# Optimization experiments

Hardware: AMD Instinct MI355X
Metric: run time of the kernel (lower is better)

The kernel has to match this reference:

```python
import jax, jax.numpy as jnp
import numpy as np

B, S, D = 2, 2048, 1024
H = 16
DH = D // H


def _layernorm(x, g, b, eps=1e-5):
    mu = jnp.mean(x, axis=-1, keepdims=True)
    var = jnp.var(x, axis=-1, keepdims=True)
    return (x - mu) * jax.lax.rsqrt(var + eps) * g + b


def setup_inputs() -> dict:
    key = jax.random.key(0)
    ks = jax.random.split(key, 8)
    s = lambda fan_in: 1.0 / np.sqrt(fan_in)
    return {
        "x": jax.random.normal(ks[0], (B, S, D), dtype=jnp.float32),
        "ln1_g": jnp.ones((D,), jnp.float32),
        "ln1_b": jnp.zeros((D,), jnp.float32),
        "w_qkv": jax.random.uniform(ks[1], (D, 3 * D), jnp.float32, -s(D), s(D)),
        "b_qkv": jnp.zeros((3 * D,), jnp.float32),
        "w_out": jax.random.uniform(ks[2], (D, D), jnp.float32, -s(D), s(D)),
        "b_out": jnp.zeros((D,), jnp.float32),
        "ln2_g": jnp.ones((D,), jnp.float32),
        "ln2_b": jnp.zeros((D,), jnp.float32),
        "w1": jax.random.uniform(ks[3], (D, 4 * D), jnp.float32, -s(D), s(D)),
        "b1": jnp.zeros((4 * D,), jnp.float32),
        "w2": jax.random.uniform(ks[4], (4 * D, D), jnp.float32, -s(4 * D), s(4 * D)),
        "b2": jnp.zeros((D,), jnp.float32),
    }


def reference(x, ln1_g, ln1_b, w_qkv, b_qkv, w_out, b_out,
              ln2_g, ln2_b, w1, b1, w2, b2):
    scale = DH ** -0.5
    residual = x
    h = _layernorm(x, ln1_g, ln1_b)
    qkv = h @ w_qkv + b_qkv                      # [B,S,3D]
    q, k, v = jnp.split(qkv, 3, axis=-1)
    # [B,S,D] -> [B,H,S,DH]
    split_heads = lambda t: t.reshape(B, S, H, DH).transpose(0, 2, 1, 3)
    q, k, v = map(split_heads, (q, k, v))
    scores = jnp.einsum("bhsd,bhtd->bhst", q, k) * scale  # full O(S^2) matrix
    attn = jax.nn.softmax(scores, axis=-1)
    out = jnp.einsum("bhst,bhtd->bhsd", attn, v)
    out = out.transpose(0, 2, 1, 3).reshape(B, S, D)
    out = out @ w_out + b_out                    # dropout is identity at eval
    x = residual + out
    residual = x
    h = _layernorm(x, ln2_g, ln2_b)
    h = jax.nn.gelu(h @ w1 + b1, approximate=False)
    h = h @ w2 + b2
    return residual + h
```

## Files before the change

### kernel.cpp

```cpp
#include <hip/hip_runtime.h>
#include <hip/hip_bf16.h>
#include <math.h>

#define Bc 2
#define Sc 2048
#define Dc 1024
#define Hc 16
#define DHc 64
#define Mc (Bc*Sc)

typedef __attribute__((ext_vector_type(8))) short bf16x8;
typedef __attribute__((ext_vector_type(4))) float f32x4;

#define QSCALE 0.18033688f

__device__ __forceinline__ ushort f2bf(float f){
  union { float f; uint32_t u; } c; c.f = f;
  uint32_t u = c.u;
  return (ushort)((u + 0x7fffu + ((u >> 16) & 1u)) >> 16);
}
__device__ __forceinline__ float fast_exp2(float x){
#if __has_builtin(__builtin_amdgcn_exp2f)
  return __builtin_amdgcn_exp2f(x);
#else
  return exp2f(x);
#endif
}
__device__ __forceinline__ float fast_rcp(float x){
#if __has_builtin(__builtin_amdgcn_rcpf)
  return __builtin_amdgcn_rcpf(x);
#else
  return 1.0f / x;
#endif
}
__device__ __forceinline__ float fast_gelu(float x){
  float x2 = x * x;
  float y  = x * (2.30220826f + 0.10294442f * x2);
  float t  = fast_exp2(fminf(y, 80.f));
  return x * t * fast_rcp(t + 1.0f);
}
__device__ __forceinline__ uint32_t cvt_pk_bf16(float a, float b){
  uint32_t r;
  asm("v_cvt_pk_bf16_f32 %0, %1, %2" : "=v"(r) : "v"(a), "v"(b));
  return r;
}

__device__ __forceinline__ void stage16(const void* g, void* lbase, int lane){
#if __has_builtin(__builtin_amdgcn_global_load_lds)
  __builtin_amdgcn_global_load_lds(
      (const __attribute__((address_space(1))) void*)g,
      (__attribute__((address_space(3))) void*)lbase, 16, 0, 0);
#else
  *(int4*)((char*)lbase + lane*16) = *(const int4*)g;
#endif
}

__global__ __launch_bounds__(256) void tcast(const float* __restrict__ w,
                                             ushort* __restrict__ wt,
                                             int K, int N){
  __shared__ float t[32][33];
  int kb = blockIdx.y * 32, nb = blockIdx.x * 32;
  int tx = threadIdx.x & 31, ty = threadIdx.x >> 5;
  #pragma unroll
  for (int i = 0; i < 4; i++)
    t[ty + 8*i][tx] = w[(size_t)(kb + ty + 8*i) * N + nb + tx];
  __syncthreads();
  #pragma unroll
  for (int i = 0; i < 4; i++)
    wt[(size_t)(nb + ty + 8*i) * K + kb + tx] = f2bf(t[tx][ty + 8*i]);
}

__global__ __launch_bounds__(256) void ln_bf16(const float* __restrict__ x,
                                               const float* __restrict__ g,
                                               const float* __restrict__ b,
                                               ushort* __restrict__ out){
  int row = blockIdx.x;
  const float4 xv = reinterpret_cast<const float4*>(x + (size_t)row * Dc)[threadIdx.x];
  float s  = xv.x + xv.y + xv.z + xv.w;
  float sq = xv.x*xv.x + xv.y*xv.y + xv.z*xv.z + xv.w*xv.w;
  #pragma unroll
  for (int m = 1; m < 64; m <<= 1){ s += __shfl_xor(s, m); sq += __shfl_xor(sq, m); }
  __shared__ float ss[4], ssq[4];
  int wv = threadIdx.x >> 6;
  if ((threadIdx.x & 63) == 0){ ss[wv] = s; ssq[wv] = sq; }
  __syncthreads();
  s  = ss[0] + ss[1] + ss[2] + ss[3];
  sq = ssq[0] + ssq[1] + ssq[2] + ssq[3];
  float mu  = s * (1.0f / Dc);
  float var = sq * (1.0f / Dc) - mu * mu;
  float rstd = rsqrtf(var + 1e-5f);
  float4 gv = reinterpret_cast<const float4*>(g)[threadIdx.x];
  float4 bv = reinterpret_cast<const float4*>(b)[threadIdx.x];
  ushort o[4];
  o[0] = f2bf((xv.x - mu) * rstd * gv.x + bv.x);
  o[1] = f2bf((xv.y - mu) * rstd * gv.y + bv.y);
  o[2] = f2bf((xv.z - mu) * rstd * gv.z + bv.z);
  o[3] = f2bf((xv.w - mu) * rstd * gv.w + bv.w);
  *reinterpret_cast<uint2*>(out + (size_t)row * Dc + threadIdx.x * 4) =
      *reinterpret_cast<uint2*>(o);
}

template<int EPI>
__global__ __launch_bounds__(256) void gemm128(
    const ushort* __restrict__ A, const ushort* __restrict__ BT,
    const float* __restrict__ bias,
    ushort* __restrict__ outb,
    ushort* __restrict__ oq, ushort* __restrict__ ok, ushort* __restrict__ ov,
    int N, int K){
  __shared__ short As[2][128*64];
  __shared__ short Bs[2][128*64];

  const int fid = blockIdx.x;
  const int q8 = gridDim.x >> 3;
  const int id2 = (fid & 7) * q8 + (fid >> 3);
  const int nbx = N / 128;
  const int nb = id2 % nbx, mb = id2 / nbx;

  const int tid = threadIdx.x;
  const int wave = tid >> 6, lane = tid & 63;
  const int wm = wave >> 1, wn = wave & 1;
  const int lr = lane & 15, lg = lane >> 4;

  f32x4 acc[4][4] = {};

  const int srow = wave * 8 + (lane >> 3);
  const int sgc  = ((lane & 7) ^ (lane >> 3)) * 8;
  const ushort* Ag = A  + (size_t)(mb * 128 + srow) * K + sgc;
  const ushort* Bg = BT + (size_t)(nb * 128 + srow) * K + sgc;
  const int nK = K >> 6;

  {
    char* Ab = (char*)&As[0][0] + wave * 1024;
    char* Bb = (char*)&Bs[0][0] + wave * 1024;
    #pragma unroll
    for (int c = 0; c < 4; c++){
      stage16(Ag + (size_t)c * 32 * K, Ab + c * 4096, lane);
      stage16(Bg + (size_t)c * 32 * K, Bb + c * 4096, lane);
    }
  }
  __syncthreads();

  const int swzr = (lr & 7) * 8;

  for (int kt = 0; kt < nK; ++kt){
    const int cur = kt & 1;
    if (kt + 1 < nK){
      const int ko = (kt + 1) * 64;
      char* Ab = (char*)&As[cur ^ 1][0] + wave * 1024;
      char* Bb = (char*)&Bs[cur ^ 1][0] + wave * 1024;
      #pragma unroll
      for (int c = 0; c < 4; c++){
        stage16(Ag + (size_t)c * 32 * K + ko, Ab + c * 4096, lane);
        stage16(Bg + (size_t)c * 32 * K + ko, Bb + c * 4096, lane);
      }
    }
    #pragma unroll
    for (int ks = 0; ks < 2; ks++){
      const int col = (ks * 32 + lg * 8) ^ swzr;
      bf16x8 af[4], bfr[4];
      #pragma unroll
      for (int mt = 0; mt < 4; mt++)
        af[mt] = *reinterpret_cast<const bf16x8*>(&As[cur][(wm*64 + mt*16 + lr)*64 + col]);
      #pragma unroll
      for (int nt = 0; nt < 4; nt++)
        bfr[nt] = *reinterpret_cast<const bf16x8*>(&Bs[cur][(wn*64 + nt*16 + lr)*64 + col]);
      #pragma unroll
      for (int mt = 0; mt < 4; mt++)
        #pragma unroll
        for (int nt = 0; nt < 4; nt++)
          acc[mt][nt] = __builtin_amdgcn_mfma_f32_16x16x32_bf16(af[mt], bfr[nt], acc[mt][nt], 0, 0, 0);
    }
    __syncthreads();
  }

  if (EPI == 0){
    #pragma unroll
    for (int mt = 0; mt < 4; mt++){
      const int gm0 = mb * 128 + wm * 64 + mt * 16 + lg * 4;
      const int bb = gm0 >> 11, s0 = gm0 & 2047;
      #pragma unroll
      for (int nt = 0; nt < 4; nt++){
        const int gn = nb * 128 + wn * 64 + nt * 16 + lr;
        const float bv = bias[gn];
        const int p = gn >> 10, d = gn & 1023;
        const int hh = d >> 6, dh = d & 63;
        const int bh = bb * Hc + hh;
        if (p == 2){
          ushort pk[4];
          #pragma unroll
          for (int r = 0; r < 4; r++) pk[r] = f2bf(acc[mt][nt][r] + bv);
          *reinterpret_cast<uint2*>(ov + ((size_t)bh * DHc + dh) * Sc + s0) =
              *reinterpret_cast<uint2*>(pk);
        } else if (p == 0){
          #pragma unroll
          for (int r = 0; r < 4; r++)
            oq[((size_t)bh * Sc + s0 + r) * DHc + dh] = f2bf((acc[mt][nt][r] + bv) * QSCALE);
        } else {
          #pragma unroll
          for (int r = 0; r < 4; r++)
            ok[((size_t)bh * Sc + s0 + r) * DHc + dh] = f2bf(acc[mt][nt][r] + bv);
        }
      }
    }
  } else {
    #pragma unroll
    for (int mt = 0; mt < 4; mt++){
      #pragma unroll
      for (int nt = 0; nt < 4; nt++){
        #pragma unroll
        for (int r = 0; r < 4; r++){
          const int gm = mb * 128 + wm * 64 + mt * 16 + lg * 4 + r;
          const int gn = nb * 128 + wn * 64 + nt * 16 + lr;
          outb[(size_t)gm * N + gn] = f2bf(fast_gelu(acc[mt][nt][r] + bias[gn]));
        }
      }
    }
  }
}

__global__ __launch_bounds__(256) void gemm_res64(
    const ushort* __restrict__ A, const ushort* __restrict__ BT,
    const float* __restrict__ bias, const float* __restrict__ res,
    float* __restrict__ outf, int N, int K){
  __shared__ short As[2][128*64];
  __shared__ short Bs[2][64*64];

  const int fid = blockIdx.x;
  const int q8 = gridDim.x >> 3;
  const int id2 = (fid & 7) * q8 + (fid >> 3);
  const int nbx = N / 64;
  const int nb = id2 % nbx, mb = id2 / nbx;

  const int tid = threadIdx.x;
  const int wave = tid >> 6, lane = tid & 63;
  const int wm = wave >> 1, wn = wave & 1;
  const int lr = lane & 15, lg = lane >> 4;

  f32x4 acc[4][2] = {};

  const int srow = wave * 8 + (lane >> 3);
  const int sgc  = ((lane & 7) ^ (lane >> 3)) * 8;
  const ushort* Ag = A  + (size_t)(mb * 128 + srow) * K + sgc;
  const ushort* Bg = BT + (size_t)(nb * 64  + srow) * K + sgc;
  const int nK = K >> 6;

  {
    char* Ab = (char*)&As[0][0] + wave * 1024;
    char* Bb = (char*)&Bs[0][0] + wave * 1024;
    #pragma unroll
    for (int c = 0; c < 4; c++)
      stage16(Ag + (size_t)c * 32 * K, Ab + c * 4096, lane);
    #pragma unroll
    for (int c = 0; c < 2; c++)
      stage16(Bg + (size_t)c * 32 * K, Bb + c * 4096, lane);
  }
  __syncthreads();

  const int swzr = (lr & 7) * 8;

  for (int kt = 0; kt < nK; ++kt){
    const int cur = kt & 1;
    if (kt + 1 < nK){
      const int ko = (kt + 1) * 64;
      char* Ab = (char*)&As[cur ^ 1][0] + wave * 1024;
      char* Bb = (char*)&Bs[cur ^ 1][0] + wave * 1024;
      #pragma unroll
      for (int c = 0; c < 4; c++)
        stage16(Ag + (size_t)c * 32 * K + ko, Ab + c * 4096, lane);
      #pragma unroll
      for (int c = 0; c < 2; c++)
        stage16(Bg + (size_t)c * 32 * K + ko, Bb + c * 4096, lane);
    }
    #pragma unroll
    for (int ks = 0; ks < 2; ks++){
      const int col = (ks * 32 + lg * 8) ^ swzr;
      bf16x8 af[4], bfr[2];
      #pragma unroll
      for (int mt = 0; mt < 4; mt++)
        af[mt] = *reinterpret_cast<const bf16x8*>(&As[cur][(wm*64 + mt*16 + lr)*64 + col]);
      #pragma unroll
      for (int nt = 0; nt < 2; nt++)
        bfr[nt] = *reinterpret_cast<const bf16x8*>(&Bs[cur][(wn*32 + nt*16 + lr)*64 + col]);
      #pragma unroll
      for (int mt = 0; mt < 4; mt++)
        #pragma unroll
        for (int nt = 0; nt < 2; nt++)
          acc[mt][nt] = __builtin_amdgcn_mfma_f32_16x16x32_bf16(af[mt], bfr[nt], acc[mt][nt], 0, 0, 0);
    }
    __syncthreads();
  }

  #pragma unroll
  for (int mt = 0; mt < 4; mt++){
    #pragma unroll
    for (int nt = 0; nt < 2; nt++){
      #pragma unroll
      for (int r = 0; r < 4; r++){
        const int gm = mb * 128 + wm * 64 + mt * 16 + lg * 4 + r;
        const int gn = nb * 64 + wn * 32 + nt * 16 + lr;
        const size_t i = (size_t)gm * N + gn;
        outf[i] = acc[mt][nt][r] + bias[gn] + res[i];
      }
    }
  }
}

__global__ __launch_bounds__(256) void flash_attn(const ushort* __restrict__ q,
                                                  const ushort* __restrict__ k,
                                                  const ushort* __restrict__ vt,
                                                  ushort* __restrict__ ctx){
  const int bh = blockIdx.x;
  const int q0 = blockIdx.y * 64;
  const int b  = bh >> 4, h = bh & 15;
  const int tid = threadIdx.x, wave = tid >> 6, lane = tid & 63;
  const int lr = lane & 15, lg = lane >> 4;

  __shared__ short Kt[2][64*64];
  __shared__ short Vt[64*64];
  __shared__ short Ps[4][16][68];

  const int g8  = lane & 7;
  const int kr0 = wave * 8 + (lane >> 3);
  const int kcol = (g8 ^ (kr0 & 7)) * 8;
  const ushort* kg0 = k + (size_t)bh * Sc * DHc + (size_t)kr0 * DHc + kcol;
  const ushort* kg1 = kg0 + 32 * DHc;
  char* Kl = (char*)&Kt[0][0] + wave * 1024;
  const int KBUFB = 64 * 64 * 2;

  const int vrow = tid >> 3, vg8 = tid & 7;
  const int vcol = (vg8 ^ (vrow & 7)) * 8;
  const ushort* vg0 = vt + (size_t)bh * DHc * Sc + (size_t)vrow * Sc + vcol;
  const ushort* vg1 = vg0 + (size_t)32 * Sc;

  bf16x8 qf0, qf1;
  {
    const ushort* qp = q + (size_t)bh * Sc * DHc + (size_t)(q0 + wave * 16 + lr) * DHc + lg * 8;
    qf0 = *reinterpret_cast<const bf16x8*>(qp);
    qf1 = *reinterpret_cast<const bf16x8*>(qp + 32);
  }

  f32x4 o[4] = {};
  float lps = 0.f;
  constexpr int NTILES = Sc / 64;

  stage16(kg0, Kl,        lane);
  stage16(kg1, Kl + 4096, lane);
  {
    int4 w0 = *reinterpret_cast<const int4*>(vg0);
    int4 w1 = *reinterpret_cast<const int4*>(vg1);
    *reinterpret_cast<int4*>((char*)&Vt[0] + tid * 16)        = w0;
    *reinterpret_cast<int4*>((char*)&Vt[0] + 4096 + tid * 16) = w1;
  }
  __syncthreads();

  const int swz = (lr & 7) * 8;

  for (int kt = 0; kt < NTILES; ++kt){
    const int cur = kt & 1;
    int4 vr0, vr1;
    if (kt + 1 < NTILES){
      const int nx = (cur ^ 1) * KBUFB;
      stage16(kg0 + (size_t)(kt + 1) * 64 * DHc, Kl + nx,        lane);
      stage16(kg1 + (size_t)(kt + 1) * 64 * DHc, Kl + nx + 4096, lane);
      vr0 = *reinterpret_cast<const int4*>(vg0 + (kt + 1) * 64);
      vr1 = *reinterpret_cast<const int4*>(vg1 + (kt + 1) * 64);
    }

    f32x4 sacc[4];
    __builtin_amdgcn_s_setprio(1);
    #pragma unroll
    for (int nt = 0; nt < 4; nt++){
      const int rb = (nt * 16 + lr) * 64;
      bf16x8 b0 = *reinterpret_cast<const bf16x8*>(&Kt[cur][rb + ((lg * 8) ^ swz)]);
      bf16x8 b1 = *reinterpret_cast<const bf16x8*>(&Kt[cur][rb + ((32 + lg * 8) ^ swz)]);
      f32x4 z = {0.f, 0.f, 0.f, 0.f};
      z = __builtin_amdgcn_mfma_f32_16x16x32_bf16(b0, qf0, z, 0, 0, 0);
      z = __builtin_amdgcn_mfma_f32_16x16x32_bf16(b1, qf1, z, 0, 0, 0);
      sacc[nt] = z;
    }
    __builtin_amdgcn_s_setprio(0);

    #pragma unroll
    for (int nt = 0; nt < 4; nt++){
      float p0 = fast_exp2(sacc[nt][0]);
      float p1 = fast_exp2(sacc[nt][1]);
      float p2 = fast_exp2(sacc[nt][2]);
      float p3 = fast_exp2(sacc[nt][3]);
      lps += (p0 + p1) + (p2 + p3);
      uint2 wd;
      wd.x = cvt_pk_bf16(p0, p1);
      wd.y = cvt_pk_bf16(p2, p3);
      *reinterpret_cast<uint2*>(&Ps[wave][lr][nt * 16 + lg * 4]) = wd;
    }

    bf16x8 pf0 = *reinterpret_cast<const bf16x8*>(&Ps[wave][lr][lg * 8]);
    bf16x8 pf1 = *reinterpret_cast<const bf16x8*>(&Ps[wave][lr][32 + lg * 8]);
    __builtin_amdgcn_s_setprio(1);
    #pragma unroll
    for (int nt = 0; nt < 4; nt++){
      const int rb = (nt * 16 + lr) * 64;
      bf16x8 v0 = *reinterpret_cast<const bf16x8*>(&Vt[rb + ((lg * 8) ^ swz)]);
      bf16x8 v1 = *reinterpret_cast<const bf16x8*>(&Vt[rb + ((32 + lg * 8) ^ swz)]);
      o[nt] = __builtin_amdgcn_mfma_f32_16x16x32_bf16(pf0, v0, o[nt], 0, 0, 0);
      o[nt] = __builtin_amdgcn_mfma_f32_16x16x32_bf16(pf1, v1, o[nt], 0, 0, 0);
    }
    __builtin_amdgcn_s_setprio(0);

    __syncthreads();
    if (kt + 1 < NTILES){
      *reinterpret_cast<int4*>((char*)&Vt[0] + tid * 16)        = vr0;
      *reinterpret_cast<int4*>((char*)&Vt[0] + 4096 + tid * 16) = vr1;
      __syncthreads();
    }
  }

  lps += __shfl_xor(lps, 16);
  lps += __shfl_xor(lps, 32);

  #pragma unroll
  for (int j = 0; j < 4; j++){
    float inv = 1.0f / __shfl(lps, lg * 4 + j);
    int s = q0 + wave * 16 + lg * 4 + j;
    ushort* op = ctx + ((size_t)b * Sc + s) * Dc + h * DHc;
    #pragma unroll
    for (int nt = 0; nt < 4; nt++)
      op[nt * 16 + lr] = f2bf(o[nt][j] * inv);
  }
}

extern "C" void kernel_launch(void* const* d_in, const int* in_sizes, int n_in,
                              void* d_out, int out_size, void* d_ws, size_t ws_size,
                              hipStream_t stream){
  const float* x     = (const float*)d_in[0];
  const float* ln1_g = (const float*)d_in[1];
  const float* ln1_b = (const float*)d_in[2];
  const float* w_qkv = (const float*)d_in[3];
  const float* b_qkv = (const float*)d_in[4];
  const float* w_out = (const float*)d_in[5];
  const float* b_out = (const float*)d_in[6];
  const float* ln2_g = (const float*)d_in[7];
  const float* ln2_b = (const float*)d_in[8];
  const float* w1    = (const float*)d_in[9];
  const float* b1    = (const float*)d_in[10];
  const float* w2    = (const float*)d_in[11];
  const float* b2    = (const float*)d_in[12];
  float* out = (float*)d_out;

  char* ws = (char*)d_ws;
  size_t off = 0;
  ushort* wqkvT = (ushort*)(ws + off); off += (size_t)3072 * 1024 * 2;
  ushort* woutT = (ushort*)(ws + off); off += (size_t)1024 * 1024 * 2;
  ushort* w1T   = (ushort*)(ws + off); off += (size_t)4096 * 1024 * 2;
  ushort* w2T   = (ushort*)(ws + off); off += (size_t)1024 * 4096 * 2;
  ushort* hln   = (ushort*)(ws + off); off += (size_t)Mc * Dc * 2;
  ushort* qbuf  = (ushort*)(ws + off); off += (size_t)32 * Sc * DHc * 2;
  ushort* kbuf  = (ushort*)(ws + off); off += (size_t)32 * Sc * DHc * 2;
  ushort* vtbuf = (ushort*)(ws + off); off += (size_t)32 * Sc * DHc * 2;
  ushort* ctx   = (ushort*)(ws + off); off += (size_t)Mc * Dc * 2;
  float*  x1    = (float*)(ws + off);  off += (size_t)Mc * Dc * 4;
  ushort* act   = qbuf;

  tcast<<<dim3(3072 / 32, 1024 / 32), 256, 0, stream>>>(w_qkv, wqkvT, 1024, 3072);
  tcast<<<dim3(1024 / 32, 1024 / 32), 256, 0, stream>>>(w_out, woutT, 1024, 1024);
  tcast<<<dim3(4096 / 32, 1024 / 32), 256, 0, stream>>>(w1,    w1T,   1024, 4096);
  tcast<<<dim3(1024 / 32, 4096 / 32), 256, 0, stream>>>(w2,    w2T,   4096, 1024);

  ln_bf16<<<Mc, 256, 0, stream>>>(x, ln1_g, ln1_b, hln);

  gemm128<0><<<(3072/128) * (Mc/128), 256, 0, stream>>>(
      hln, wqkvT, b_qkv, nullptr, qbuf, kbuf, vtbuf, 3072, 1024);

  flash_attn<<<dim3(32, Sc / 64), 256, 0, stream>>>(qbuf, kbuf, vtbuf, ctx);

  gemm_res64<<<(1024/64) * (Mc/128), 256, 0, stream>>>(
      ctx, woutT, b_out, x, x1, 1024, 1024);

  ln_bf16<<<Mc, 256, 0, stream>>>(x1, ln2_g, ln2_b, hln);

  gemm128<2><<<(4096/128) * (Mc/128), 256, 0, stream>>>(
      hln, w1T, b1, act, nullptr, nullptr, nullptr, 4096, 1024);

  gemm_res64<<<(1024/64) * (Mc/128), 256, 0, stream>>>(
      act, w2T, b2, x1, out, 1024, 4096);
}
```

Baseline: 248.0 us.

## Permute V layout to feed P from registers, double-buffer V tile

The QKV GEMM epilogue now stores V^T columns within each 64-key block in a permuted order, so the P accumulator registers from the QK^T MFMA can serve directly as the A operand of the PV MFMA. This removes the per-wave LDS round trip for P. V is also double-buffered in shared memory, and the next tile is written before the PV MFMAs, which drops one __syncthreads per iteration. The cost is that correctness now depends on the permutation matching the MFMA register layout exactly, and the kernel uses an extra 8KB of LDS for the second V buffer.

```diff
diff --git a/kernel.cpp b/kernel.cpp
--- a/kernel.cpp
+++ b/kernel.cpp
@@ -189,7 +189,10 @@
           ushort pk[4];
           #pragma unroll
           for (int r = 0; r < 4; r++) pk[r] = f2bf(acc[mt][nt][r] + bv);
-          *reinterpret_cast<uint2*>(ov + ((size_t)bh * DHc + dh) * Sc + s0) =
+          const int blk = s0 >> 6;
+          const int local = s0 & 63;
+          const int pos = (local & 32) + ((local & 12) << 1) + ((local & 16) >> 2);
+          *reinterpret_cast<uint2*>(ov + ((size_t)bh * DHc + dh) * Sc + blk * 64 + pos) =
               *reinterpret_cast<uint2*>(pk);
         } else if (p == 0){
           #pragma unroll
@@ -316,8 +319,7 @@
   const int lr = lane & 15, lg = lane >> 4;
 
   __shared__ short Kt[2][64*64];
-  __shared__ short Vt[64*64];
-  __shared__ short Ps[4][16][68];
+  __shared__ short Vt[2][64*64];
 
   const int g8  = lane & 7;
   const int kr0 = wave * 8 + (lane >> 3);
@@ -348,8 +350,8 @@
   {
     int4 w0 = *reinterpret_cast<const int4*>(vg0);
     int4 w1 = *reinterpret_cast<const int4*>(vg1);
-    *reinterpret_cast<int4*>((char*)&Vt[0] + tid * 16)        = w0;
-    *reinterpret_cast<int4*>((char*)&Vt[0] + 4096 + tid * 16) = w1;
+    *reinterpret_cast<int4*>((char*)&Vt[0][0] + tid * 16)        = w0;
+    *reinterpret_cast<int4*>((char*)&Vt[0][0] + 4096 + tid * 16) = w1;
   }
   __syncthreads();
 
@@ -380,6 +382,7 @@
     }
     __builtin_amdgcn_s_setprio(0);
 
+    uint32_t W[4][2];
     #pragma unroll
     for (int nt = 0; nt < 4; nt++){
       float p0 = fast_exp2(sacc[nt][0]);
@@ -387,31 +390,32 @@
       float p2 = fast_exp2(sacc[nt][2]);
       float p3 = fast_exp2(sacc[nt][3]);
       lps += (p0 + p1) + (p2 + p3);
-      uint2 wd;
-      wd.x = cvt_pk_bf16(p0, p1);
-      wd.y = cvt_pk_bf16(p2, p3);
-      *reinterpret_cast<uint2*>(&Ps[wave][lr][nt * 16 + lg * 4]) = wd;
-    }
-
-    bf16x8 pf0 = *reinterpret_cast<const bf16x8*>(&Ps[wave][lr][lg * 8]);
-    bf16x8 pf1 = *reinterpret_cast<const bf16x8*>(&Ps[wave][lr][32 + lg * 8]);
+      W[nt][0] = cvt_pk_bf16(p0, p1);
+      W[nt][1] = cvt_pk_bf16(p2, p3);
+    }
+
+    if (kt + 1 < NTILES){
+      *reinterpret_cast<int4*>((char*)&Vt[cur ^ 1][0] + tid * 16)        = vr0;
+      *reinterpret_cast<int4*>((char*)&Vt[cur ^ 1][0] + 4096 + tid * 16) = vr1;
+    }
+
+    union { uint32_t u[4]; bf16x8 v; } c0, c1;
+    c0.u[0] = W[0][0]; c0.u[1] = W[0][1]; c0.u[2] = W[1][0]; c0.u[3] = W[1][1];
+    c1.u[0] = W[2][0]; c1.u[1] = W[2][1]; c1.u[2] = W[3][0]; c1.u[3] = W[3][1];
+    bf16x8 pf0 = c0.v, pf1 = c1.v;
+
     __builtin_amdgcn_s_setprio(1);
     #pragma unroll
     for (int nt = 0; nt < 4; nt++){
       const int rb = (nt * 16 + lr) * 64;
-      bf16x8 v0 = *reinterpret_cast<const bf16x8*>(&Vt[rb + ((lg * 8) ^ swz)]);
-      bf16x8 v1 = *reinterpret_cast<const bf16x8*>(&Vt[rb + ((32 + lg * 8) ^ swz)]);
+      bf16x8 v0 = *reinterpret_cast<const bf16x8*>(&Vt[cur][rb + ((lg * 8) ^ swz)]);
+      bf16x8 v1 = *reinterpret_cast<const bf16x8*>(&Vt[cur][rb + ((32 + lg * 8) ^ swz)]);
       o[nt] = __builtin_amdgcn_mfma_f32_16x16x32_bf16(pf0, v0, o[nt], 0, 0, 0);
       o[nt] = __builtin_amdgcn_mfma_f32_16x16x32_bf16(pf1, v1, o[nt], 0, 0, 0);
     }
     __builtin_amdgcn_s_setprio(0);
 
     __syncthreads();
-    if (kt + 1 < NTILES){
-      *reinterpret_cast<int4*>((char*)&Vt[0] + tid * 16)        = vr0;
-      *reinterpret_cast<int4*>((char*)&Vt[0] + 4096 + tid * 16) = vr1;
-      __syncthreads();
-    }
   }
 
   lps += __shfl_xor(lps, 16);
```

Result: no change. 246.4 us (-0.6%).
